# Performance work log

Hardware: AMD Instinct MI355X
Metric: run time of the kernel (lower is better)

Reference implementation:

```python
import jax, jax.numpy as jnp
import numpy as np

IN_FEATURES = 4096
OUT_FEATURES = 4096
BANDWIDTH = min(IN_FEATURES, OUT_FEATURES) // 8  # 512, as in the torch default


def band_indices(n_out, n_in, bw):
    """Vectorized equivalent of BandMatrix.create_band_indices (COO row/col lists)."""
    i = np.arange(n_out)
    lo = np.maximum(0, i - bw)
    hi = np.minimum(n_in, i + bw + 1)
    counts = hi - lo
    total = int(counts.sum())
    rows = np.repeat(i, counts)
    start = np.cumsum(counts) - counts  # offset of each row's first entry
    cols = np.arange(total) - np.repeat(start, counts) + np.repeat(lo, counts)
    return rows.astype(np.int32), cols.astype(np.int32)


def setup_inputs() -> dict:
    key = jax.random.key(0)
    kx, kw = jax.random.split(key)
    rows_np, cols_np = band_indices(OUT_FEATURES, IN_FEATURES, BANDWIDTH)
    nnz = rows_np.shape[0]  # 3935744
    x = jax.random.normal(kx, (4, 2048, IN_FEATURES), dtype=jnp.float32)
    W_values = jax.random.normal(kw, (nnz,), dtype=jnp.float32)
    bias = jnp.zeros((OUT_FEATURES,), dtype=jnp.float32)
    return {
        "x": x,
        "W_values": W_values,
        "bias": bias,
        "rows": jnp.asarray(rows_np),
        "cols": jnp.asarray(cols_np),
    }


def reference(x, W_values, bias, rows, cols):
    # Densify banded COO weight [out, in] (matches sparse_coo_tensor().to_dense()).
    W = jnp.zeros((OUT_FEATURES, IN_FEATURES), dtype=W_values.dtype).at[rows, cols].set(W_values)
    # x: [B, S, in] @ W.T: [in, out] -> [B, S, out]
    out = jnp.einsum('bsi,oi->bso', x, W) + bias
    return out
```

## Files before the change

### kernel.cpp

```cpp
#include <hip/hip_runtime.h>
#include <stdint.h>

#define IN_F  4096
#define OUT_F 4096
#define BW    512
#define WB2   1280
#define BM    256
#define BN    256

typedef __bf16 bf16x8 __attribute__((ext_vector_type(8)));
typedef float  f32x4  __attribute__((ext_vector_type(4)));

__device__ __forceinline__ int band_start(int o) {
    if (o <= 512)  return o * 513 + ((o * (o - 1)) >> 1);
    if (o <= 3584) return 393472 + (o - 512) * 1025;
    const int d = o - 3584;
    return 3542272 + (((1024 + 4609 - o) * d) >> 1);
}

__device__ __forceinline__ uint16_t f32_to_bf16(float f) {
    uint32_t u = __builtin_bit_cast(uint32_t, f);
    u += 0x7FFFu + ((u >> 16) & 1u);
    return (uint16_t)(u >> 16);
}

__global__ __launch_bounds__(256) void cvt_x(const float* __restrict__ x,
                                             uint16_t* __restrict__ xb, int n4) {
    const int stride = gridDim.x * 256;
    for (int i = blockIdx.x * 256 + threadIdx.x; i < n4; i += stride) {
        const float4 v = reinterpret_cast<const float4*>(x)[i];
        const uint32_t lo = (uint32_t)f32_to_bf16(v.x) | ((uint32_t)f32_to_bf16(v.y) << 16);
        const uint32_t hi = (uint32_t)f32_to_bf16(v.z) | ((uint32_t)f32_to_bf16(v.w) << 16);
        reinterpret_cast<uint2*>(xb)[i] = make_uint2(lo, hi);
    }
}

__global__ __launch_bounds__(256) void cvt_w(const float* __restrict__ wv,
                                             uint16_t* __restrict__ wd) {
    const int o = blockIdx.y;
    const int j = blockIdx.x * 256 + threadIdx.x;
    const int i = (o & ~(BM - 1)) - BW + j;
    uint16_t v = 0;
    if (i >= o - BW && i <= o + BW && i >= 0 && i < IN_F) {
        const int lo = (o > BW) ? (o - BW) : 0;
        v = f32_to_bf16(wv[band_start(o) + (i - lo)]);
    }
    wd[o * WB2 + j] = v;
}

__global__ __launch_bounds__(512, 1) void band_gemm_v7(
    const uint16_t* __restrict__ xb,
    const uint16_t* __restrict__ wd,
    const float* __restrict__ bias,
    float* __restrict__ out)
{
    __shared__ __align__(128) uint8_t lds[131072];

    const int id  = blockIdx.x;
    const int xcd = id & 7;
    const int r   = id >> 3;
    const int bx  = 2 * xcd + (r & 1);
    const int by  = r >> 1;
    const int brow = by * BM;
    const int bcol = bx * BN;

    const int wlo    = bcol - BW;
    const int kstart = wlo > 0 ? wlo : 0;
    const int kend   = (bcol + BN + BW) < IN_F ? (bcol + BN + BW) : IN_F;
    const int nt     = (kend - kstart) >> 6;
    const int j0     = kstart - wlo;

    const int tid  = threadIdx.x;
    const int w    = tid >> 6;
    const int lane = tid & 63;
    const int ln   = lane & 15;
    const int kc   = lane >> 4;
    const int wm   = w >> 2;
    const int wn   = w & 3;

    const int srow = tid >> 3;
    const int csrc = (tid & 7) ^ (srow & 7);
    const uint16_t* aSrc = xb + (size_t)(brow + srow) * IN_F + kstart + csrc * 8;
    const uint16_t* bSrc = wd + (size_t)(bcol + srow) * WB2 + j0 + csrc * 8;

#define GLOAD(srcp, dst_off)                                                             \
    __builtin_amdgcn_global_load_lds(                                                    \
        (const __attribute__((address_space(1))) uint32_t*)(srcp),                       \
        (__attribute__((address_space(3))) uint32_t*)(lds + (dst_off) + (w << 10)),      \
        16, 0, 0)

#define STAGE(ts_, sb_) {                                                                \
        const uint16_t* as_ = aSrc + (ts_) * 64;                                         \
        const uint16_t* bs_ = bSrc + (ts_) * 64;                                         \
        GLOAD(as_,                        (sb_) + 0);                                    \
        GLOAD(as_ + (size_t)64  * IN_F,   (sb_) + 8192);                                 \
        GLOAD(as_ + (size_t)128 * IN_F,   (sb_) + 16384);                                \
        GLOAD(as_ + (size_t)192 * IN_F,   (sb_) + 24576);                                \
        GLOAD(bs_,                        (sb_) + 32768);                                \
        GLOAD(bs_ + (size_t)64  * WB2,    (sb_) + 40960);                                \
        GLOAD(bs_ + (size_t)128 * WB2,    (sb_) + 49152);                                \
        GLOAD(bs_ + (size_t)192 * WB2,    (sb_) + 57344); }

    const int cswz = (kc ^ (ln & 7)) << 4;
    int aOff[8], bOff[4];
    #pragma unroll
    for (int a = 0; a < 8; ++a) aOff[a] = ((wm * 128 + a * 16 + ln) << 7) + cswz;
    #pragma unroll
    for (int n = 0; n < 4; ++n) bOff[n] = 32768 + ((wn * 64 + n * 16 + ln) << 7) + cswz;

    bf16x8 a0[4][2], a1[4][2], b0[2][2], b1[2][2];

#define LD_A(DST, BB, MQ) {                                                              \
    _Pragma("unroll")                                                                    \
    for (int a_ = 0; a_ < 4; ++a_) {                                                     \
        DST[a_][0] = *(const bf16x8*)(lds + (BB) + aOff[(MQ) * 4 + a_]);                 \
        DST[a_][1] = *(const bf16x8*)(lds + (BB) + (aOff[(MQ) * 4 + a_] ^ 64));          \
    } }
#define LD_B(DST, BB, NQ) {                                                              \
    _Pragma("unroll")                                                                    \
    for (int n_ = 0; n_ < 2; ++n_) {                                                     \
        DST[n_][0] = *(const bf16x8*)(lds + (BB) + bOff[(NQ) * 2 + n_]);                 \
        DST[n_][1] = *(const bf16x8*)(lds + (BB) + (bOff[(NQ) * 2 + n_] ^ 64));          \
    } }
#define MFMAQ(AF, BF, MQ, NQ) {                                                          \
    __builtin_amdgcn_s_setprio(1);                                                       \
    _Pragma("unroll")                                                                    \
    for (int a_ = 0; a_ < 4; ++a_) {                                                     \
        _Pragma("unroll")                                                                \
        for (int n_ = 0; n_ < 2; ++n_) {                                                 \
            acc[(MQ)*4+a_][(NQ)*2+n_] = __builtin_amdgcn_mfma_f32_16x16x32_bf16(         \
                AF[a_][0], BF[n_][0], acc[(MQ)*4+a_][(NQ)*2+n_], 0, 0, 0);               \
            acc[(MQ)*4+a_][(NQ)*2+n_] = __builtin_amdgcn_mfma_f32_16x16x32_bf16(         \
                AF[a_][1], BF[n_][1], acc[(MQ)*4+a_][(NQ)*2+n_], 0, 0, 0);               \
        } }                                                                              \
    __builtin_amdgcn_s_setprio(0); }

    f32x4 acc[8][4] = {};

    STAGE(0, 0);
    STAGE(1, 65536);
    asm volatile("s_waitcnt vmcnt(8)" ::: "memory");
    __builtin_amdgcn_s_barrier();
    LD_A(a0, 0, 0);
    LD_B(b1, 0, 1);

    for (int v = 0; v < nt; ++v) {
        const int cur = (v & 1) << 16;
        const int nxt = cur ^ 65536;

        LD_B(b0, cur, 0);
        LD_A(a1, cur, 1);
        MFMAQ(a0, b0, 0, 0);

        MFMAQ(a0, b1, 0, 1);
        asm volatile("s_waitcnt vmcnt(0)" ::: "memory");
        __builtin_amdgcn_s_barrier();

        if (v + 1 < nt) LD_A(a0, nxt, 0);
        MFMAQ(a1, b1, 1, 1);
        __builtin_amdgcn_s_barrier();
        __builtin_amdgcn_sched_barrier(0);

        if (v + 2 < nt) STAGE(v + 2, cur);
        if (v + 1 < nt) LD_B(b1, nxt, 1);
        MFMAQ(a1, b0, 1, 0);
    }
#undef STAGE
#undef GLOAD

    const int ocol = bcol + wn * 64 + ln;
    float bsv[4];
    #pragma unroll
    for (int n = 0; n < 4; ++n) bsv[n] = bias[ocol + n * 16];

    #pragma unroll
    for (int a = 0; a < 8; ++a) {
        #pragma unroll
        for (int q = 0; q < 4; ++q) {
            const int row = brow + wm * 128 + a * 16 + (kc << 2) + q;
            float* po = out + (size_t)row * OUT_F + ocol;
            #pragma unroll
            for (int n = 0; n < 4; ++n)
                po[n * 16] = acc[a][n][q] + bsv[n];
        }
    }
}

__global__ __launch_bounds__(256) void band_gemm_f32(
    const float* __restrict__ x, const float* __restrict__ wv,
    const float* __restrict__ bias, float* __restrict__ out, int M)
{
    __shared__ float Xs[128][33];
    __shared__ float Ws[32][130];
    const int tid = threadIdx.x;
    const int tx = tid & 15, ty = tid >> 4;
    const int bcol = blockIdx.x * 128, brow = blockIdx.y * 128;
    const int klo = (bcol >= BW) ? (bcol - BW) : 0;
    const int khi = min(IN_F, bcol + 128 + BW);
    float acc[8][8];
    #pragma unroll
    for (int a = 0; a < 8; ++a)
        #pragma unroll
        for (int b = 0; b < 8; ++b) acc[a][b] = 0.f;
    const int xc4 = (tid & 7) * 4, xr0 = tid >> 3;
    const int wc = tid & 31, wr0 = tid >> 5;
    for (int k0 = klo; k0 < khi; k0 += 32) {
        #pragma unroll
        for (int p = 0; p < 4; ++p) {
            const int rr = xr0 + 32 * p;
            const float4 v = *reinterpret_cast<const float4*>(&x[(size_t)(brow + rr) * IN_F + (k0 + xc4)]);
            Xs[rr][xc4 + 0] = v.x; Xs[rr][xc4 + 1] = v.y; Xs[rr][xc4 + 2] = v.z; Xs[rr][xc4 + 3] = v.w;
        }
        const int i = k0 + wc;
        #pragma unroll
        for (int p = 0; p < 16; ++p) {
            const int rr = wr0 + 8 * p;
            const int o = bcol + rr;
            const int lo = (o >= BW) ? (o - BW) : 0;
            float v = 0.f;
            if (i >= o - BW && i <= o + BW) v = wv[band_start(o) + (i - lo)];
            Ws[wc][rr] = v;
        }
        __syncthreads();
        #pragma unroll
        for (int k = 0; k < 32; ++k) {
            float am[8];
            #pragma unroll
            for (int a = 0; a < 8; ++a) am[a] = Xs[ty * 8 + a][k];
            float bo[8];
            #pragma unroll
            for (int b = 0; b < 4; ++b) { bo[b] = Ws[k][tx * 4 + b]; bo[4 + b] = Ws[k][tx * 4 + 64 + b]; }
            #pragma unroll
            for (int a = 0; a < 8; ++a)
                #pragma unroll
                for (int b = 0; b < 8; ++b) acc[a][b] = fmaf(am[a], bo[b], acc[a][b]);
        }
        __syncthreads();
    }
    #pragma unroll
    for (int a = 0; a < 8; ++a) {
        const size_t row = (size_t)(brow + ty * 8 + a);
        #pragma unroll
        for (int b = 0; b < 4; ++b) {
            out[row * OUT_F + bcol + tx * 4 + b]      = acc[a][b]     + bias[bcol + tx * 4 + b];
            out[row * OUT_F + bcol + tx * 4 + 64 + b] = acc[a][4 + b] + bias[bcol + tx * 4 + 64 + b];
        }
    }
}

extern "C" void kernel_launch(void* const* d_in, const int* in_sizes, int n_in,
                              void* d_out, int out_size, void* d_ws, size_t ws_size,
                              hipStream_t stream) {
    const float* x    = (const float*)d_in[0];
    const float* wv   = (const float*)d_in[1];
    const float* bias = (const float*)d_in[2];
    float* out        = (float*)d_out;

    const int M = in_sizes[0] / IN_F;
    const size_t xb_bytes = (size_t)M * IN_F * 2;
    const size_t wd_bytes = (size_t)OUT_F * WB2 * 2;

    if (ws_size >= xb_bytes + wd_bytes && (M % BM) == 0) {
        uint16_t* xb  = (uint16_t*)d_ws;
        uint16_t* wdp = (uint16_t*)((uint8_t*)d_ws + xb_bytes);
        cvt_x<<<2048, 256, 0, stream>>>(x, xb, M * IN_F / 4);
        cvt_w<<<dim3(WB2 / 256, OUT_F), 256, 0, stream>>>(wv, wdp);
        band_gemm_v7<<<(M / BM) * (OUT_F / BN), 512, 0, stream>>>(xb, wdp, bias, out);
    } else {
        dim3 grid(OUT_F / 128, M / 128);
        band_gemm_f32<<<grid, 256, 0, stream>>>(x, wv, bias, out, M);
    }
}
```

Measured before the change: 143.1 us.

## Load banded weight fragments directly into registers, stage only activations via LDS

New measurement: 186.2 us. 30.1% more time.

```diff
diff --git a/kernel.cpp b/kernel.cpp
--- a/kernel.cpp
+++ b/kernel.cpp
@@ -48,7 +48,7 @@
     wd[o * WB2 + j] = v;
 }
 
-__global__ __launch_bounds__(512, 1) void band_gemm_v7(
+__global__ __launch_bounds__(512, 1) void band_gemm_v8(
     const uint16_t* __restrict__ xb,
     const uint16_t* __restrict__ wd,
     const float* __restrict__ bias,
@@ -81,7 +81,6 @@
     const int srow = tid >> 3;
     const int csrc = (tid & 7) ^ (srow & 7);
     const uint16_t* aSrc = xb + (size_t)(brow + srow) * IN_F + kstart + csrc * 8;
-    const uint16_t* bSrc = wd + (size_t)(bcol + srow) * WB2 + j0 + csrc * 8;
 
 #define GLOAD(srcp, dst_off)                                                             \
     __builtin_amdgcn_global_load_lds(                                                    \
@@ -89,83 +88,81 @@
         (__attribute__((address_space(3))) uint32_t*)(lds + (dst_off) + (w << 10)),      \
         16, 0, 0)
 
-#define STAGE(ts_, sb_) {                                                                \
-        const uint16_t* as_ = aSrc + (ts_) * 64;                                         \
-        const uint16_t* bs_ = bSrc + (ts_) * 64;                                         \
-        GLOAD(as_,                        (sb_) + 0);                                    \
-        GLOAD(as_ + (size_t)64  * IN_F,   (sb_) + 8192);                                 \
-        GLOAD(as_ + (size_t)128 * IN_F,   (sb_) + 16384);                                \
-        GLOAD(as_ + (size_t)192 * IN_F,   (sb_) + 24576);                                \
-        GLOAD(bs_,                        (sb_) + 32768);                                \
-        GLOAD(bs_ + (size_t)64  * WB2,    (sb_) + 40960);                                \
-        GLOAD(bs_ + (size_t)128 * WB2,    (sb_) + 49152);                                \
-        GLOAD(bs_ + (size_t)192 * WB2,    (sb_) + 57344); }
+#define STAGE_A(v_, slot_) { const uint16_t* as_ = aSrc + (v_) * 64;                     \
+        GLOAD(as_,                        (slot_) * 32768 + 0);                          \
+        GLOAD(as_ + (size_t)64  * IN_F,   (slot_) * 32768 + 8192);                       \
+        GLOAD(as_ + (size_t)128 * IN_F,   (slot_) * 32768 + 16384);                      \
+        GLOAD(as_ + (size_t)192 * IN_F,   (slot_) * 32768 + 24576); }
+
+    const uint16_t* bPtr = wd + (size_t)(bcol + wn * 64 + ln) * WB2 + j0 + kc * 8;
+
+#define LOADB(DST, v_) {                                                                 \
+    _Pragma("unroll")                                                                    \
+    for (int n_ = 0; n_ < 4; ++n_) {                                                     \
+        _Pragma("unroll")                                                                \
+        for (int ks_ = 0; ks_ < 2; ++ks_)                                                \
+            DST[n_][ks_] = *(const bf16x8*)(bPtr + (size_t)n_ * 16 * WB2 + (v_) * 64 + ks_ * 32); \
+    } }
 
     const int cswz = (kc ^ (ln & 7)) << 4;
-    int aOff[8], bOff[4];
+    int aOff[8];
     #pragma unroll
     for (int a = 0; a < 8; ++a) aOff[a] = ((wm * 128 + a * 16 + ln) << 7) + cswz;
-    #pragma unroll
-    for (int n = 0; n < 4; ++n) bOff[n] = 32768 + ((wn * 64 + n * 16 + ln) << 7) + cswz;
-
-    bf16x8 a0[4][2], a1[4][2], b0[2][2], b1[2][2];
-
-#define LD_A(DST, BB, MQ) {                                                              \
+
+#define COMPUTE(BB, SB) {                                                                \
     _Pragma("unroll")                                                                    \
-    for (int a_ = 0; a_ < 4; ++a_) {                                                     \
-        DST[a_][0] = *(const bf16x8*)(lds + (BB) + aOff[(MQ) * 4 + a_]);                 \
-        DST[a_][1] = *(const bf16x8*)(lds + (BB) + (aOff[(MQ) * 4 + a_] ^ 64));          \
+    for (int mq = 0; mq < 2; ++mq) {                                                     \
+        bf16x8 af[4][2];                                                                 \
+        _Pragma("unroll")                                                                \
+        for (int a_ = 0; a_ < 4; ++a_) {                                                 \
+            af[a_][0] = *(const bf16x8*)(lds + (SB) + aOff[mq * 4 + a_]);                \
+            af[a_][1] = *(const bf16x8*)(lds + (SB) + (aOff[mq * 4 + a_] ^ 64));         \
+        }                                                                                \
+        __builtin_amdgcn_s_setprio(1);                                                   \
+        _Pragma("unroll")                                                                \
+        for (int a_ = 0; a_ < 4; ++a_) {                                                 \
+            _Pragma("unroll")                                                            \
+            for (int n_ = 0; n_ < 4; ++n_) {                                             \
+                acc[mq * 4 + a_][n_] = __builtin_amdgcn_mfma_f32_16x16x32_bf16(          \
+                    af[a_][0], BB[n_][0], acc[mq * 4 + a_][n_], 0, 0, 0);                \
+                acc[mq * 4 + a_][n_] = __builtin_amdgcn_mfma_f32_16x16x32_bf16(          \
+                    af[a_][1], BB[n_][1], acc[mq * 4 + a_][n_], 0, 0, 0);                \
+            } }                                                                          \
+        __builtin_amdgcn_s_setprio(0);                                                   \
     } }
-#define LD_B(DST, BB, NQ) {                                                              \
-    _Pragma("unroll")                                                                    \
-    for (int n_ = 0; n_ < 2; ++n_) {                                                     \
-        DST[n_][0] = *(const bf16x8*)(lds + (BB) + bOff[(NQ) * 2 + n_]);                 \
-        DST[n_][1] = *(const bf16x8*)(lds + (BB) + (bOff[(NQ) * 2 + n_] ^ 64));          \
-    } }
-#define MFMAQ(AF, BF, MQ, NQ) {                                                          \
-    __builtin_amdgcn_s_setprio(1);                                                       \
-    _Pragma("unroll")                                                                    \
-    for (int a_ = 0; a_ < 4; ++a_) {                                                     \
-        _Pragma("unroll")                                                                \
-        for (int n_ = 0; n_ < 2; ++n_) {                                                 \
-            acc[(MQ)*4+a_][(NQ)*2+n_] = __builtin_amdgcn_mfma_f32_16x16x32_bf16(         \
-                AF[a_][0], BF[n_][0], acc[(MQ)*4+a_][(NQ)*2+n_], 0, 0, 0);               \
-            acc[(MQ)*4+a_][(NQ)*2+n_] = __builtin_amdgcn_mfma_f32_16x16x32_bf16(         \
-                AF[a_][1], BF[n_][1], acc[(MQ)*4+a_][(NQ)*2+n_], 0, 0, 0);               \
-        } }                                                                              \
-    __builtin_amdgcn_s_setprio(0); }
+
+#define TILE_END(cond_)                                                                  \
+    if (cond_) { asm volatile("s_waitcnt vmcnt(4)" ::: "memory"); }                      \
+    else       { asm volatile("s_waitcnt vmcnt(0)" ::: "memory"); }                      \
+    __builtin_amdgcn_s_barrier();                                                        \
+    asm volatile("" ::: "memory");
 
     f32x4 acc[8][4] = {};
-
-    STAGE(0, 0);
-    STAGE(1, 65536);
-    asm volatile("s_waitcnt vmcnt(8)" ::: "memory");
+    bf16x8 bEv[4][2], bOd[4][2];
+
+    LOADB(bEv, 0);
+    STAGE_A(0, 0);
+    STAGE_A(1, 1);
+    asm volatile("s_waitcnt vmcnt(4)" ::: "memory");
     __builtin_amdgcn_s_barrier();
-    LD_A(a0, 0, 0);
-    LD_B(b1, 0, 1);
-
-    for (int v = 0; v < nt; ++v) {
-        const int cur = (v & 1) << 16;
-        const int nxt = cur ^ 65536;
-
-        LD_B(b0, cur, 0);
-        LD_A(a1, cur, 1);
-        MFMAQ(a0, b0, 0, 0);
-
-        MFMAQ(a0, b1, 0, 1);
-        asm volatile("s_waitcnt vmcnt(0)" ::: "memory");
-        __builtin_amdgcn_s_barrier();
-
-        if (v + 1 < nt) LD_A(a0, nxt, 0);
-        MFMAQ(a1, b1, 1, 1);
-        __builtin_amdgcn_s_barrier();
+    asm volatile("" ::: "memory");
+
+    const int nt2 = nt >> 1;
+    for (int t = 0; t < nt2; ++t) {
+        const int v0 = 2 * t;
+        const int s0 = (t & 1) << 1;
+        LOADB(bOd, v0 + 1);
+        if (v0 + 2 < nt) STAGE_A(v0 + 2, s0 ^ 2);
         __builtin_amdgcn_sched_barrier(0);
-
-        if (v + 2 < nt) STAGE(v + 2, cur);
-        if (v + 1 < nt) LD_B(b1, nxt, 1);
-        MFMAQ(a1, b0, 1, 0);
-    }
-#undef STAGE
+        COMPUTE(bEv, s0 * 32768);
+        TILE_END(v0 + 2 < nt);
+        if (v0 + 2 < nt) LOADB(bEv, v0 + 2);
+        if (v0 + 3 < nt) STAGE_A(v0 + 3, (s0 ^ 2) + 1);
+        __builtin_amdgcn_sched_barrier(0);
+        COMPUTE(bOd, (s0 + 1) * 32768);
+        TILE_END(v0 + 3 < nt);
+    }
+#undef STAGE_A
 #undef GLOAD
 
     const int ocol = bcol + wn * 64 + ln;
@@ -265,7 +262,7 @@
         uint16_t* wdp = (uint16_t*)((uint8_t*)d_ws + xb_bytes);
         cvt_x<<<2048, 256, 0, stream>>>(x, xb, M * IN_F / 4);
         cvt_w<<<dim3(WB2 / 256, OUT_F), 256, 0, stream>>>(wv, wdp);
-        band_gemm_v7<<<(M / BM) * (OUT_F / BN), 512, 0, stream>>>(xb, wdp, bias, out);
+        band_gemm_v8<<<(M / BM) * (OUT_F / BN), 512, 0, stream>>>(xb, wdp, bias, out);
     } else {
         dim3 grid(OUT_F / 128, M / 128);
         band_gemm_f32<<<grid, 256, 0, stream>>>(x, wv, bias, out, M);
```

## Replace double-buffered K tiles with nine-slot ring of quarter-tile LDS units

Applied to the files above, without the earlier changes.

Measured after the change: 140.4 us. Within noise of the previous version (-1.9%).

```diff
diff --git a/kernel.cpp b/kernel.cpp
--- a/kernel.cpp
+++ b/kernel.cpp
@@ -48,13 +48,13 @@
     wd[o * WB2 + j] = v;
 }
 
-__global__ __launch_bounds__(512, 1) void band_gemm_v7(
+__global__ __launch_bounds__(512, 1) void band_gemm_v9(
     const uint16_t* __restrict__ xb,
     const uint16_t* __restrict__ wd,
     const float* __restrict__ bias,
     float* __restrict__ out)
 {
-    __shared__ __align__(128) uint8_t lds[131072];
+    __shared__ __align__(128) uint8_t lds[9 * 16384];
 
     const int id  = blockIdx.x;
     const int xcd = id & 7;
@@ -89,83 +89,87 @@
         (__attribute__((address_space(3))) uint32_t*)(lds + (dst_off) + (w << 10)),      \
         16, 0, 0)
 
-#define STAGE(ts_, sb_) {                                                                \
-        const uint16_t* as_ = aSrc + (ts_) * 64;                                         \
-        const uint16_t* bs_ = bSrc + (ts_) * 64;                                         \
-        GLOAD(as_,                        (sb_) + 0);                                    \
-        GLOAD(as_ + (size_t)64  * IN_F,   (sb_) + 8192);                                 \
-        GLOAD(as_ + (size_t)128 * IN_F,   (sb_) + 16384);                                \
-        GLOAD(as_ + (size_t)192 * IN_F,   (sb_) + 24576);                                \
-        GLOAD(bs_,                        (sb_) + 32768);                                \
-        GLOAD(bs_ + (size_t)64  * WB2,    (sb_) + 40960);                                \
-        GLOAD(bs_ + (size_t)128 * WB2,    (sb_) + 49152);                                \
-        GLOAD(bs_ + (size_t)192 * WB2,    (sb_) + 57344); }
+#define STG_UNIT(w_, j_, slot_) {                                                        \
+        if (((j_) & 1) == 0) {                                                           \
+            const uint16_t* p_ = aSrc + (size_t)(((j_) >> 1) * 128) * IN_F + (w_) * 64;  \
+            GLOAD(p_, (slot_) << 14);                                                    \
+            GLOAD(p_ + (size_t)64 * IN_F, ((slot_) << 14) + 8192);                       \
+        } else {                                                                         \
+            const uint16_t* p_ = bSrc + (size_t)(((j_) >> 1) * 128) * WB2 + (w_) * 64;   \
+            GLOAD(p_, (slot_) << 14);                                                    \
+            GLOAD(p_ + (size_t)64 * WB2, ((slot_) << 14) + 8192);                        \
+        } }
 
     const int cswz = (kc ^ (ln & 7)) << 4;
-    int aOff[8], bOff[4];
-    #pragma unroll
-    for (int a = 0; a < 8; ++a) aOff[a] = ((wm * 128 + a * 16 + ln) << 7) + cswz;
-    #pragma unroll
-    for (int n = 0; n < 4; ++n) bOff[n] = 32768 + ((wn * 64 + n * 16 + ln) << 7) + cswz;
-
-    bf16x8 a0[4][2], a1[4][2], b0[2][2], b1[2][2];
-
-#define LD_A(DST, BB, MQ) {                                                              \
+
+#define LD_A(BASE, MQ) {                                                                 \
     _Pragma("unroll")                                                                    \
-    for (int a_ = 0; a_ < 4; ++a_) {                                                     \
-        DST[a_][0] = *(const bf16x8*)(lds + (BB) + aOff[(MQ) * 4 + a_]);                 \
-        DST[a_][1] = *(const bf16x8*)(lds + (BB) + (aOff[(MQ) * 4 + a_] ^ 64));          \
+    for (int s_ = 0; s_ < 4; ++s_) {                                                     \
+        const int off_ = (BASE) + (((MQ) * 64 + s_ * 16 + ln) << 7) + cswz;              \
+        am[s_][0] = *(const bf16x8*)(lds + off_);                                        \
+        am[s_][1] = *(const bf16x8*)(lds + (off_ ^ 64));                                 \
     } }
-#define LD_B(DST, BB, NQ) {                                                              \
+#define LD_B(DST, BASE, NQ) {                                                            \
     _Pragma("unroll")                                                                    \
-    for (int n_ = 0; n_ < 2; ++n_) {                                                     \
-        DST[n_][0] = *(const bf16x8*)(lds + (BB) + bOff[(NQ) * 2 + n_]);                 \
-        DST[n_][1] = *(const bf16x8*)(lds + (BB) + (bOff[(NQ) * 2 + n_] ^ 64));          \
+    for (int s_ = 0; s_ < 2; ++s_) {                                                     \
+        const int off_ = (BASE) + (((wn & 1) * 64 + (NQ) * 32 + s_ * 16 + ln) << 7) + cswz; \
+        DST[s_][0] = *(const bf16x8*)(lds + off_);                                       \
+        DST[s_][1] = *(const bf16x8*)(lds + (off_ ^ 64));                                \
     } }
-#define MFMAQ(AF, BF, MQ, NQ) {                                                          \
+#define MFMAPH(MROW, NCOL, BB) {                                                         \
     __builtin_amdgcn_s_setprio(1);                                                       \
     _Pragma("unroll")                                                                    \
     for (int a_ = 0; a_ < 4; ++a_) {                                                     \
         _Pragma("unroll")                                                                \
         for (int n_ = 0; n_ < 2; ++n_) {                                                 \
-            acc[(MQ)*4+a_][(NQ)*2+n_] = __builtin_amdgcn_mfma_f32_16x16x32_bf16(         \
-                AF[a_][0], BF[n_][0], acc[(MQ)*4+a_][(NQ)*2+n_], 0, 0, 0);               \
-            acc[(MQ)*4+a_][(NQ)*2+n_] = __builtin_amdgcn_mfma_f32_16x16x32_bf16(         \
-                AF[a_][1], BF[n_][1], acc[(MQ)*4+a_][(NQ)*2+n_], 0, 0, 0);               \
+            acc[(MROW) + a_][(NCOL) + n_] = __builtin_amdgcn_mfma_f32_16x16x32_bf16(     \
+                am[a_][0], BB[n_][0], acc[(MROW) + a_][(NCOL) + n_], 0, 0, 0);           \
+            acc[(MROW) + a_][(NCOL) + n_] = __builtin_amdgcn_mfma_f32_16x16x32_bf16(     \
+                am[a_][1], BB[n_][1], acc[(MROW) + a_][(NCOL) + n_], 0, 0, 0);           \
         } }                                                                              \
     __builtin_amdgcn_s_setprio(0); }
 
     f32x4 acc[8][4] = {};
-
-    STAGE(0, 0);
-    STAGE(1, 65536);
-    asm volatile("s_waitcnt vmcnt(8)" ::: "memory");
+    bf16x8 am[4][2], bn0[2][2], bn1[2][2];
+
+    STG_UNIT(0, 0, 0); STG_UNIT(0, 1, 1); STG_UNIT(0, 2, 2); STG_UNIT(0, 3, 3);
+    STG_UNIT(1, 0, 4);
+    asm volatile("s_waitcnt vmcnt(2)" ::: "memory");
     __builtin_amdgcn_s_barrier();
-    LD_A(a0, 0, 0);
-    LD_B(b1, 0, 1);
-
+
+    int s4v = 0;
     for (int v = 0; v < nt; ++v) {
-        const int cur = (v & 1) << 16;
-        const int nxt = cur ^ 65536;
-
-        LD_B(b0, cur, 0);
-        LD_A(a1, cur, 1);
-        MFMAQ(a0, b0, 0, 0);
-
-        MFMAQ(a0, b1, 0, 1);
-        asm volatile("s_waitcnt vmcnt(0)" ::: "memory");
-        __builtin_amdgcn_s_barrier();
-
-        if (v + 1 < nt) LD_A(a0, nxt, 0);
-        MFMAQ(a1, b1, 1, 1);
-        __builtin_amdgcn_s_barrier();
-        __builtin_amdgcn_sched_barrier(0);
-
-        if (v + 2 < nt) STAGE(v + 2, cur);
-        if (v + 1 < nt) LD_B(b1, nxt, 1);
-        MFMAQ(a1, b0, 1, 0);
-    }
-#undef STAGE
+        int sA = s4v + (wm << 1);           if (sA >= 9) sA -= 9;
+        int sB = s4v + 1 + ((wn >> 1) << 1); if (sB >= 9) sB -= 9;
+        const int aBase = sA << 14, bBase = sB << 14;
+        int st0 = s4v + 5; if (st0 >= 9) st0 -= 9;
+        int st1 = st0 + 1; if (st1 >= 9) st1 -= 9;
+        int st2 = st1 + 1; if (st2 >= 9) st2 -= 9;
+        int st3 = st2 + 1; if (st3 >= 9) st3 -= 9;
+        const bool stg_q012 = (v + 1 < nt);
+        const bool stg_q3   = (v + 2 < nt);
+
+        LD_A(aBase, 0);
+        LD_B(bn0, bBase, 0);
+        if (stg_q012) STG_UNIT(v + 1, 1, st0);
+        MFMAPH(0, 0, bn0);
+        LD_B(bn1, bBase, 1);
+        if (stg_q012) STG_UNIT(v + 1, 2, st1);
+        MFMAPH(0, 2, bn1);
+        LD_A(aBase, 1);
+        if (stg_q012) STG_UNIT(v + 1, 3, st2);
+        MFMAPH(4, 2, bn1);
+        if (stg_q3) STG_UNIT(v + 2, 0, st3);
+        MFMAPH(4, 0, bn0);
+
+        if (v + 1 < nt) {
+            if (v + 2 < nt) { asm volatile("s_waitcnt vmcnt(2)" ::: "memory"); }
+            else            { asm volatile("s_waitcnt vmcnt(0)" ::: "memory"); }
+            __builtin_amdgcn_s_barrier();
+        }
+        s4v += 4; if (s4v >= 9) s4v -= 9;
+    }
+#undef STG_UNIT
 #undef GLOAD
 
     const int ocol = bcol + wn * 64 + ln;
@@ -224,16 +228,16 @@
         __syncthreads();
         #pragma unroll
         for (int k = 0; k < 32; ++k) {
-            float am[8];
-            #pragma unroll
-            for (int a = 0; a < 8; ++a) am[a] = Xs[ty * 8 + a][k];
+            float amv[8];
+            #pragma unroll
+            for (int a = 0; a < 8; ++a) amv[a] = Xs[ty * 8 + a][k];
             float bo[8];
             #pragma unroll
             for (int b = 0; b < 4; ++b) { bo[b] = Ws[k][tx * 4 + b]; bo[4 + b] = Ws[k][tx * 4 + 64 + b]; }
             #pragma unroll
             for (int a = 0; a < 8; ++a)
                 #pragma unroll
-                for (int b = 0; b < 8; ++b) acc[a][b] = fmaf(am[a], bo[b], acc[a][b]);
+                for (int b = 0; b < 8; ++b) acc[a][b] = fmaf(amv[a], bo[b], acc[a][b]);
         }
         __syncthreads();
     }
@@ -265,7 +269,7 @@
         uint16_t* wdp = (uint16_t*)((uint8_t*)d_ws + xb_bytes);
         cvt_x<<<2048, 256, 0, stream>>>(x, xb, M * IN_F / 4);
         cvt_w<<<dim3(WB2 / 256, OUT_F), 256, 0, stream>>>(wv, wdp);
-        band_gemm_v7<<<(M / BM) * (OUT_F / BN), 512, 0, stream>>>(xb, wdp, bias, out);
+        band_gemm_v9<<<(M / BM) * (OUT_F / BN), 512, 0, stream>>>(xb, wdp, bias, out);
     } else {
         dim3 grid(OUT_F / 128, M / 128);
         band_gemm_f32<<<grid, 256, 0, stream>>>(x, wv, bias, out, M);
```
